# Kernel optimization log

Hardware: AMD Instinct MI355X
Metric: run time of the kernel (lower is better)

The kernel has to match this reference:

```python
import jax, jax.numpy as jnp
import numpy as np

B, N = 4096, 8192
PULSE_LO = 40.0 / 60.0   # Hz
PULSE_HI = 250.0 / 60.0  # Hz


def setup_inputs() -> dict:
    key = jax.random.key(0)
    k1, k2 = jax.random.split(key)
    outputs = jax.random.normal(k1, (B, N), dtype=jnp.float32)
    # reference heart rates in Hz, uniform inside the pulse band
    targets = jax.random.uniform(k2, (B, 1), dtype=jnp.float32,
                                 minval=PULSE_LO, maxval=PULSE_HI)
    return {"outputs": outputs, "targets": targets, "Fs": 20}


def reference(outputs, targets, Fs):
    n = outputs.shape[-1]
    F = n // 2 + 1
    f = jnp.linspace(0.0, Fs / 2.0, F, dtype=jnp.float32)  # [F]

    min_idx = jnp.argmin(jnp.abs(f - PULSE_LO))
    max_idx = jnp.argmin(jnp.abs(f - PULSE_HI))

    # normalized rFFT power spectrum (torch.rfft(..., normalized=True) divides by sqrt(N))
    X = jnp.fft.rfft(outputs) * (1.0 / np.sqrt(n))          # [B, F] complex
    P1 = X.real ** 2 + X.imag ** 2                          # [B, F]

    # per-sample reference bin index
    r = jnp.argmin(jnp.abs(f[None, :] - targets.reshape(-1, 1)), axis=1)  # [B]
    rb = r[:, None]                                         # [B, 1]
    i = jnp.arange(F)[None, :]                              # [1, F]

    # signal mask u: 1 at ref and 1st harmonic, 0.5 at ref+-1 (applied after, as in torch)
    u = jnp.where((i == rb - 1) | (i == rb + 1), 0.5,
                  jnp.where((i == rb) | (i == 2 * rb), 1.0, 0.0))
    # noise mask w = 1 - u, zeroed outside pulse band and around 1st harmonic
    w = jnp.where((i < min_idx) | (i >= max_idx) |
                  (i == 2 * rb - 1) | (i == 2 * rb + 1),
                  0.0, 1.0 - u)

    signal_energy = jnp.sum(P1 * u, axis=1)                 # [B]
    noise_energy = jnp.sum(P1 * w, axis=1)                  # [B]
    losses = -10.0 * jnp.log(signal_energy / (noise_energy + 1.0)) / jnp.log(10.0)
    return jnp.mean(losses)
```

## Files before the change

### kernel.cpp

```cpp
#include <hip/hip_runtime.h>
#include <math.h>

#define TPB 256

typedef float cplx __attribute__((ext_vector_type(2)));

__device__ __forceinline__ cplx cmul(cplx a, cplx b) {
    return a.xx * b + cplx{-a.y, a.y} * b.yx;
}

__device__ __forceinline__ void dft4(cplx& a, cplx& b, cplx& c, cplx& d) {
    cplx t0 = a + c, t1 = a - c, t2 = b + d, t3 = b - d;
    a = t0 + t2;
    c = t0 - t2;
    cplx jt3 = cplx{t3.y, -t3.x};
    b = t1 + jt3;
    d = t1 - jt3;
}

#define T16(j) (4 * ((j) & 3) + ((j) >> 2))

__device__ __forceinline__ void dft16(cplx v[16]) {
#pragma unroll
    for (int j = 0; j < 4; ++j) dft4(v[j], v[4 + j], v[8 + j], v[12 + j]);
    const float C1 = 0.9238795325112867f, S1 = 0.3826834323650898f;
    const float R2 = 0.7071067811865476f;
    v[5]  = cmul(v[5],  cplx{ C1, -S1});
    v[9]  = cmul(v[9],  cplx{ R2, -R2});
    v[13] = cmul(v[13], cplx{ S1, -C1});
    v[6]  = cmul(v[6],  cplx{ R2, -R2});
    v[10] = cplx{v[10].y, -v[10].x};
    v[14] = cmul(v[14], cplx{-R2, -R2});
    v[7]  = cmul(v[7],  cplx{ S1, -C1});
    v[11] = cmul(v[11], cplx{-R2, -R2});
    v[15] = cmul(v[15], cplx{-C1,  S1});
#pragma unroll
    for (int b = 0; b < 4; ++b) dft4(v[4 * b], v[4 * b + 1], v[4 * b + 2], v[4 * b + 3]);
}

__global__ __launch_bounds__(TPB, 4) void snr_kernel(const float* __restrict__ x,
                                                     const float* __restrict__ targets,
                                                     float* __restrict__ out) {
    __shared__ __align__(16) cplx Z[4096];
    float* zf = (float*)Z;

    const int t = threadIdx.x;
    const int blk = blockIdx.x;
    const int tl = t & 15;

    int r;
    {
        float tg = targets[blk];
        const float df = 0.00244140625f;
        int c0 = (int)(tg * 409.6f) - 2;
        if (c0 < 0) c0 = 0;
        r = c0;
        float best = fabsf(df * (float)c0 - tg);
        for (int i = c0 + 1; i <= c0 + 4 && i <= 4096; ++i) {
            float dd = fabsf(df * (float)i - tg);
            if (dd < best) { best = dd; r = i; }
        }
    }

    cplx a[16];
    const cplx* row = (const cplx*)(x + (size_t)blk * 8192);
#pragma unroll
    for (int l = 0; l < 16; ++l) a[l] = row[t + 256 * l];

    dft16(a);
    {
        float ang = -1.5339807878856412e-3f * (float)t;
        float sn, cs; __sincosf(ang, &sn, &cs);
        cplx w1 = cplx{cs, sn};
        cplx w2 = cmul(w1, w1), w3 = cmul(w2, w1);
        cplx w4 = cmul(w2, w2), w8 = cmul(w4, w4), w12 = cmul(w8, w4);
        cplx wa[4] = {cplx{1.f, 0.f}, w1, w2, w3};
        cplx wb[4] = {cplx{1.f, 0.f}, w4, w8, w12};
#pragma unroll
        for (int m = 1; m < 16; ++m) {
            int j = T16(m);
            a[j] = cmul(a[j], cmul(wb[m >> 2], wa[m & 3]));
        }
    }
    {
        const int wb0 = t << 4;
#pragma unroll
        for (int j = 0; j < 16; ++j) Z[wb0 + (T16(j) ^ tl)] = a[j];
    }
    __syncthreads();

    const int rb = t ^ ((t >> 4) & 15);
#pragma unroll
    for (int l = 0; l < 16; ++l) a[l] = Z[rb + (l << 8)];
    __syncthreads();
    dft16(a);
    {
        const int p = t >> 4;
        float ang = -0.02454369260617026f * (float)p;
        float sn, cs; __sincosf(ang, &sn, &cs);
        cplx w1 = cplx{cs, sn};
        cplx w2 = cmul(w1, w1), w3 = cmul(w2, w1);
        cplx w4 = cmul(w2, w2), w8 = cmul(w4, w4), w12 = cmul(w8, w4);
        cplx wa[4] = {cplx{1.f, 0.f}, w1, w2, w3};
        cplx wb[4] = {cplx{1.f, 0.f}, w4, w8, w12};
#pragma unroll
        for (int m = 1; m < 16; ++m) {
            int j = T16(m);
            a[j] = cmul(a[j], cmul(wb[m >> 2], wa[m & 3]));
        }
    }
    {
        const int base1 = (t >> 4) << 8;
#pragma unroll
        for (int m = 0; m < 16; ++m) {
            Z[base1 + (m << 4) + (tl ^ m)] = a[T16(m)];
        }
    }
    __syncthreads();

#pragma unroll
    for (int l = 0; l < 16; ++l) a[l] = Z[rb + (l << 8)];
    __syncthreads();
    dft16(a);

    {
        const int wb0 = t << 4;
#pragma unroll
        for (int j = 0; j < 16; ++j) Z[wb0 + (T16(j) ^ tl)] = a[j];
    }
    __syncthreads();

    float band = 0.f;
    {
        float ang = -7.669903939428206e-4f * (float)t;
        float sn, cs; __sincosf(ang, &sn, &cs);
        cplx wku = cplx{cs, sn};
        const float WCc[7] = {1.f, 0.9807852804032304f, 0.9238795325112867f,
                              0.8314696123025452f, 0.7071067811865476f,
                              0.5555702330196022f, 0.3826834323650898f};
        const float WCs[7] = {0.f, -0.19509032201612825f, -0.3826834323650898f,
                              -0.5555702330196022f, -0.7071067811865476f,
                              -0.8314696123025452f, -0.9238795325112867f};
        const int pc = ((256 - t) & 255) << 4;
        const int pl = (16 - tl) & 15;
#pragma unroll
        for (int m = 1; m <= 6; ++m) {
            const int k = t + (m << 8);
            const int za = t ? (pc | ((15 - m) ^ pl)) : (16 - m);
            cplx Zk = a[T16(m)];
            cplx Zn = Z[za];
            cplx wk = cmul(wku, cplx{WCc[m], WCs[m]});
            cplx Znc = cplx{Zn.x, -Zn.y};
            cplx s  = Zk + Znc;
            cplx dd = Zk - Znc;
            cplx tt = cmul(wk, dd);
            cplx X  = s + cplx{tt.y, -tt.x};
            float P = (X.x * X.x + X.y * X.y) * (1.0f / 32768.0f);
            if ((unsigned)(k - 273) <= 1433u) band += P;
        }
    }

    float capP = 0.f;
    if (t < 6) {
        const int c = (t < 3) ? (r - 1 + t) : (2 * r - 4 + t);
        const int kk = (c <= 2048) ? c : (4096 - c);
        const int nb = (4096 - kk) & 4095;
        const int zka = ((kk & 255) << 4) | ((kk >> 8) ^ (kk & 15));
        const int zna = ((nb & 255) << 4) | ((nb >> 8) ^ (nb & 15));
        cplx Zk = Z[zka], Zn = Z[zna];
        float ang = -7.669903939428206e-4f * (float)kk;
        float sn, cs; __sincosf(ang, &sn, &cs);
        cplx wk = cplx{cs, sn};
        cplx Znc = cplx{Zn.x, -Zn.y};
        cplx s  = Zk + Znc;
        cplx dd = Zk - Znc;
        cplx tt = cmul(wk, dd);
        cplx X  = (c <= 2048) ? (s + cplx{tt.y, -tt.x})
                              : (s + cplx{-tt.y, tt.x});
        capP = (X.x * X.x + X.y * X.y) * (1.0f / 32768.0f);
    }
    __syncthreads();

    if (t < 6) zf[t] = capP;

#pragma unroll
    for (int off = 32; off > 0; off >>= 1) band += __shfl_down(band, off);
    if ((t & 63) == 0) zf[8 + (t >> 6)] = band;
    __syncthreads();

    if (t == 0) {
        float bb = zf[8] + zf[9] + zf[10] + zf[11];
        float S = zf[1] + zf[4] + 0.5f * (zf[0] + zf[2]);
        float noise = bb;
        const int r2 = 2 * r;
        if (r <= 1706)      noise -= zf[1];
        if (r - 1 >= 273)   noise -= 0.5f * zf[0];
        if (r + 1 <= 1706)  noise -= 0.5f * zf[2];
        if (r2 - 1 <= 1706) noise -= zf[3];
        if (r2 <= 1706)     noise -= zf[4];
        if (r2 + 1 <= 1706) noise -= zf[5];
        float loss = -10.0f * log10f(S / (noise + 1.0f));
        atomicAdd(out, loss * (1.0f / 4096.0f));
    }
}

extern "C" void kernel_launch(void* const* d_in, const int* in_sizes, int n_in,
                              void* d_out, int out_size, void* d_ws, size_t ws_size,
                              hipStream_t stream) {
    const float* x = (const float*)d_in[0];
    const float* tg = (const float*)d_in[1];
    float* out = (float*)d_out;
    hipMemsetAsync(out, 0, sizeof(float), stream);
    snr_kernel<<<4096, TPB, 0, stream>>>(x, tg, out);
}
```

Before: 209.2 us.

## Process four rows per block with register prefetch of next row

Each block now handles four consecutive rows, loading the next row's input into a register buffer while the current row's FFT and band reductions run. Loss values are accumulated per block, so only one atomic add is issued per block. This aims to hide global load latency and cut launch and atomic overhead. In exchange it adds 32 live VGPRs for the prefetch buffer, with a risk of spills or lower occupancy, and it reduces the grid to a quarter of the blocks.

After: 288.7 us. +38.0%, slower.

```diff
diff --git a/kernel.cpp b/kernel.cpp
--- a/kernel.cpp
+++ b/kernel.cpp
@@ -2,6 +2,7 @@
 #include <math.h>
 
 #define TPB 256
+#define ROWS 4
 
 typedef float cplx __attribute__((ext_vector_type(2)));
 
@@ -45,163 +46,176 @@
     float* zf = (float*)Z;
 
     const int t = threadIdx.x;
-    const int blk = blockIdx.x;
     const int tl = t & 15;
-
-    int r;
+    const int rb = t ^ ((t >> 4) & 15);
+    const int wb0 = t << 4;
+    const int row0 = blockIdx.x * ROWS;
+
+    cplx a[16], pf[16];
     {
-        float tg = targets[blk];
-        const float df = 0.00244140625f;
-        int c0 = (int)(tg * 409.6f) - 2;
-        if (c0 < 0) c0 = 0;
-        r = c0;
-        float best = fabsf(df * (float)c0 - tg);
-        for (int i = c0 + 1; i <= c0 + 4 && i <= 4096; ++i) {
-            float dd = fabsf(df * (float)i - tg);
-            if (dd < best) { best = dd; r = i; }
-        }
+        const cplx* rowp = (const cplx*)(x + (size_t)row0 * 8192);
+#pragma unroll
+        for (int l = 0; l < 16; ++l) a[l] = rowp[t + 256 * l];
     }
 
-    cplx a[16];
-    const cplx* row = (const cplx*)(x + (size_t)blk * 8192);
-#pragma unroll
-    for (int l = 0; l < 16; ++l) a[l] = row[t + 256 * l];
-
-    dft16(a);
-    {
-        float ang = -1.5339807878856412e-3f * (float)t;
-        float sn, cs; __sincosf(ang, &sn, &cs);
-        cplx w1 = cplx{cs, sn};
-        cplx w2 = cmul(w1, w1), w3 = cmul(w2, w1);
-        cplx w4 = cmul(w2, w2), w8 = cmul(w4, w4), w12 = cmul(w8, w4);
-        cplx wa[4] = {cplx{1.f, 0.f}, w1, w2, w3};
-        cplx wb[4] = {cplx{1.f, 0.f}, w4, w8, w12};
-#pragma unroll
-        for (int m = 1; m < 16; ++m) {
-            int j = T16(m);
-            a[j] = cmul(a[j], cmul(wb[m >> 2], wa[m & 3]));
-        }
-    }
-    {
-        const int wb0 = t << 4;
+    float lossSum = 0.f;
+
+    for (int it = 0; it < ROWS; ++it) {
+        if (it + 1 < ROWS) {
+            const cplx* rowp = (const cplx*)(x + (size_t)(row0 + it + 1) * 8192);
+#pragma unroll
+            for (int l = 0; l < 16; ++l) pf[l] = rowp[t + 256 * l];
+        }
+
+        int r;
+        {
+            float tg = targets[row0 + it];
+            const float df = 0.00244140625f;
+            int c0 = (int)(tg * 409.6f) - 2;
+            if (c0 < 0) c0 = 0;
+            r = c0;
+            float best = fabsf(df * (float)c0 - tg);
+            for (int i = c0 + 1; i <= c0 + 4 && i <= 4096; ++i) {
+                float dd = fabsf(df * (float)i - tg);
+                if (dd < best) { best = dd; r = i; }
+            }
+        }
+
+        dft16(a);
+        {
+            float ang = -1.5339807878856412e-3f * (float)t;
+            float sn, cs; __sincosf(ang, &sn, &cs);
+            cplx w1 = cplx{cs, sn};
+            cplx w2 = cmul(w1, w1), w3 = cmul(w2, w1);
+            cplx w4 = cmul(w2, w2), w8 = cmul(w4, w4), w12 = cmul(w8, w4);
+            cplx wa[4] = {cplx{1.f, 0.f}, w1, w2, w3};
+            cplx wb[4] = {cplx{1.f, 0.f}, w4, w8, w12};
+#pragma unroll
+            for (int m = 1; m < 16; ++m) {
+                int j = T16(m);
+                a[j] = cmul(a[j], cmul(wb[m >> 2], wa[m & 3]));
+            }
+        }
 #pragma unroll
         for (int j = 0; j < 16; ++j) Z[wb0 + (T16(j) ^ tl)] = a[j];
-    }
-    __syncthreads();
-
-    const int rb = t ^ ((t >> 4) & 15);
-#pragma unroll
-    for (int l = 0; l < 16; ++l) a[l] = Z[rb + (l << 8)];
-    __syncthreads();
-    dft16(a);
-    {
-        const int p = t >> 4;
-        float ang = -0.02454369260617026f * (float)p;
-        float sn, cs; __sincosf(ang, &sn, &cs);
-        cplx w1 = cplx{cs, sn};
-        cplx w2 = cmul(w1, w1), w3 = cmul(w2, w1);
-        cplx w4 = cmul(w2, w2), w8 = cmul(w4, w4), w12 = cmul(w8, w4);
-        cplx wa[4] = {cplx{1.f, 0.f}, w1, w2, w3};
-        cplx wb[4] = {cplx{1.f, 0.f}, w4, w8, w12};
-#pragma unroll
-        for (int m = 1; m < 16; ++m) {
-            int j = T16(m);
-            a[j] = cmul(a[j], cmul(wb[m >> 2], wa[m & 3]));
-        }
-    }
-    {
-        const int base1 = (t >> 4) << 8;
-#pragma unroll
-        for (int m = 0; m < 16; ++m) {
-            Z[base1 + (m << 4) + (tl ^ m)] = a[T16(m)];
-        }
-    }
-    __syncthreads();
-
-#pragma unroll
-    for (int l = 0; l < 16; ++l) a[l] = Z[rb + (l << 8)];
-    __syncthreads();
-    dft16(a);
-
-    {
-        const int wb0 = t << 4;
+        __syncthreads();
+
+#pragma unroll
+        for (int l = 0; l < 16; ++l) a[l] = Z[rb + (l << 8)];
+        __syncthreads();
+        dft16(a);
+        {
+            const int p = t >> 4;
+            float ang = -0.02454369260617026f * (float)p;
+            float sn, cs; __sincosf(ang, &sn, &cs);
+            cplx w1 = cplx{cs, sn};
+            cplx w2 = cmul(w1, w1), w3 = cmul(w2, w1);
+            cplx w4 = cmul(w2, w2), w8 = cmul(w4, w4), w12 = cmul(w8, w4);
+            cplx wa[4] = {cplx{1.f, 0.f}, w1, w2, w3};
+            cplx wb[4] = {cplx{1.f, 0.f}, w4, w8, w12};
+#pragma unroll
+            for (int m = 1; m < 16; ++m) {
+                int j = T16(m);
+                a[j] = cmul(a[j], cmul(wb[m >> 2], wa[m & 3]));
+            }
+        }
+        {
+            const int base1 = (t >> 4) << 8;
+#pragma unroll
+            for (int m = 0; m < 16; ++m) {
+                Z[base1 + (m << 4) + (tl ^ m)] = a[T16(m)];
+            }
+        }
+        __syncthreads();
+
+#pragma unroll
+        for (int l = 0; l < 16; ++l) a[l] = Z[rb + (l << 8)];
+        __syncthreads();
+        dft16(a);
+
 #pragma unroll
         for (int j = 0; j < 16; ++j) Z[wb0 + (T16(j) ^ tl)] = a[j];
-    }
-    __syncthreads();
-
-    float band = 0.f;
-    {
-        float ang = -7.669903939428206e-4f * (float)t;
-        float sn, cs; __sincosf(ang, &sn, &cs);
-        cplx wku = cplx{cs, sn};
-        const float WCc[7] = {1.f, 0.9807852804032304f, 0.9238795325112867f,
-                              0.8314696123025452f, 0.7071067811865476f,
-                              0.5555702330196022f, 0.3826834323650898f};
-        const float WCs[7] = {0.f, -0.19509032201612825f, -0.3826834323650898f,
-                              -0.5555702330196022f, -0.7071067811865476f,
-                              -0.8314696123025452f, -0.9238795325112867f};
-        const int pc = ((256 - t) & 255) << 4;
-        const int pl = (16 - tl) & 15;
-#pragma unroll
-        for (int m = 1; m <= 6; ++m) {
-            const int k = t + (m << 8);
-            const int za = t ? (pc | ((15 - m) ^ pl)) : (16 - m);
-            cplx Zk = a[T16(m)];
-            cplx Zn = Z[za];
-            cplx wk = cmul(wku, cplx{WCc[m], WCs[m]});
+        __syncthreads();
+
+        float band = 0.f;
+        {
+            float ang = -7.669903939428206e-4f * (float)t;
+            float sn, cs; __sincosf(ang, &sn, &cs);
+            cplx wku = cplx{cs, sn};
+            const float WCc[7] = {1.f, 0.9807852804032304f, 0.9238795325112867f,
+                                  0.8314696123025452f, 0.7071067811865476f,
+                                  0.5555702330196022f, 0.3826834323650898f};
+            const float WCs[7] = {0.f, -0.19509032201612825f, -0.3826834323650898f,
+                                  -0.5555702330196022f, -0.7071067811865476f,
+                                  -0.8314696123025452f, -0.9238795325112867f};
+            const int pc = ((256 - t) & 255) << 4;
+            const int pl = (16 - tl) & 15;
+#pragma unroll
+            for (int m = 1; m <= 6; ++m) {
+                const int k = t + (m << 8);
+                const int za = t ? (pc | ((15 - m) ^ pl)) : (16 - m);
+                cplx Zk = a[T16(m)];
+                cplx Zn = Z[za];
+                cplx wk = cmul(wku, cplx{WCc[m], WCs[m]});
+                cplx Znc = cplx{Zn.x, -Zn.y};
+                cplx s  = Zk + Znc;
+                cplx dd = Zk - Znc;
+                cplx tt = cmul(wk, dd);
+                cplx X  = s + cplx{tt.y, -tt.x};
+                float P = (X.x * X.x + X.y * X.y) * (1.0f / 32768.0f);
+                if ((unsigned)(k - 273) <= 1433u) band += P;
+            }
+        }
+
+        float capP = 0.f;
+        if (t < 6) {
+            const int c = (t < 3) ? (r - 1 + t) : (2 * r - 4 + t);
+            const int kk = (c <= 2048) ? c : (4096 - c);
+            const int nb = (4096 - kk) & 4095;
+            const int zka = ((kk & 255) << 4) | ((kk >> 8) ^ (kk & 15));
+            const int zna = ((nb & 255) << 4) | ((nb >> 8) ^ (nb & 15));
+            cplx Zk = Z[zka], Zn = Z[zna];
+            float ang = -7.669903939428206e-4f * (float)kk;
+            float sn, cs; __sincosf(ang, &sn, &cs);
+            cplx wk = cplx{cs, sn};
             cplx Znc = cplx{Zn.x, -Zn.y};
             cplx s  = Zk + Znc;
             cplx dd = Zk - Znc;
             cplx tt = cmul(wk, dd);
-            cplx X  = s + cplx{tt.y, -tt.x};
-            float P = (X.x * X.x + X.y * X.y) * (1.0f / 32768.0f);
-            if ((unsigned)(k - 273) <= 1433u) band += P;
+            cplx X  = (c <= 2048) ? (s + cplx{tt.y, -tt.x})
+                                  : (s + cplx{-tt.y, tt.x});
+            capP = (X.x * X.x + X.y * X.y) * (1.0f / 32768.0f);
+        }
+        __syncthreads();
+
+        if (t < 6) zf[t] = capP;
+
+#pragma unroll
+        for (int off = 32; off > 0; off >>= 1) band += __shfl_down(band, off);
+        if ((t & 63) == 0) zf[8 + (t >> 6)] = band;
+        __syncthreads();
+
+        if (t == 0) {
+            float bb = zf[8] + zf[9] + zf[10] + zf[11];
+            float S = zf[1] + zf[4] + 0.5f * (zf[0] + zf[2]);
+            float noise = bb;
+            const int r2 = 2 * r;
+            if (r <= 1706)      noise -= zf[1];
+            if (r - 1 >= 273)   noise -= 0.5f * zf[0];
+            if (r + 1 <= 1706)  noise -= 0.5f * zf[2];
+            if (r2 - 1 <= 1706) noise -= zf[3];
+            if (r2 <= 1706)     noise -= zf[4];
+            if (r2 + 1 <= 1706) noise -= zf[5];
+            lossSum += -10.0f * log10f(S / (noise + 1.0f));
+        }
+
+        if (it + 1 < ROWS) {
+#pragma unroll
+            for (int l = 0; l < 16; ++l) a[l] = pf[l];
         }
     }
 
-    float capP = 0.f;
-    if (t < 6) {
-        const int c = (t < 3) ? (r - 1 + t) : (2 * r - 4 + t);
-        const int kk = (c <= 2048) ? c : (4096 - c);
-        const int nb = (4096 - kk) & 4095;
-        const int zka = ((kk & 255) << 4) | ((kk >> 8) ^ (kk & 15));
-        const int zna = ((nb & 255) << 4) | ((nb >> 8) ^ (nb & 15));
-        cplx Zk = Z[zka], Zn = Z[zna];
-        float ang = -7.669903939428206e-4f * (float)kk;
-        float sn, cs; __sincosf(ang, &sn, &cs);
-        cplx wk = cplx{cs, sn};
-        cplx Znc = cplx{Zn.x, -Zn.y};
-        cplx s  = Zk + Znc;
-        cplx dd = Zk - Znc;
-        cplx tt = cmul(wk, dd);
-        cplx X  = (c <= 2048) ? (s + cplx{tt.y, -tt.x})
-                              : (s + cplx{-tt.y, tt.x});
-        capP = (X.x * X.x + X.y * X.y) * (1.0f / 32768.0f);
-    }
-    __syncthreads();
-
-    if (t < 6) zf[t] = capP;
-
-#pragma unroll
-    for (int off = 32; off > 0; off >>= 1) band += __shfl_down(band, off);
-    if ((t & 63) == 0) zf[8 + (t >> 6)] = band;
-    __syncthreads();
-
-    if (t == 0) {
-        float bb = zf[8] + zf[9] + zf[10] + zf[11];
-        float S = zf[1] + zf[4] + 0.5f * (zf[0] + zf[2]);
-        float noise = bb;
-        const int r2 = 2 * r;
-        if (r <= 1706)      noise -= zf[1];
-        if (r - 1 >= 273)   noise -= 0.5f * zf[0];
-        if (r + 1 <= 1706)  noise -= 0.5f * zf[2];
-        if (r2 - 1 <= 1706) noise -= zf[3];
-        if (r2 <= 1706)     noise -= zf[4];
-        if (r2 + 1 <= 1706) noise -= zf[5];
-        float loss = -10.0f * log10f(S / (noise + 1.0f));
-        atomicAdd(out, loss * (1.0f / 4096.0f));
-    }
+    if (t == 0) atomicAdd(out, lossSum * (1.0f / 4096.0f));
 }
 
 extern "C" void kernel_launch(void* const* d_in, const int* in_sizes, int n_in,
@@ -211,5 +225,5 @@
     const float* tg = (const float*)d_in[1];
     float* out = (float*)d_out;
     hipMemsetAsync(out, 0, sizeof(float), stream);
-    snr_kernel<<<4096, TPB, 0, stream>>>(x, tg, out);
-}
+    snr_kernel<<<4096 / ROWS, TPB, 0, stream>>>(x, tg, out);
+}
```
